# Kernel tuning notes

Measured on AMD Instinct MI355X. Metric: run time of the kernel, lower is better.

Reference implementation:

```python
import jax, jax.numpy as jnp
import numpy as np

N = 50000      # nodes
E = 800000     # edges (avg degree 16)
D = 128        # in_dim
H = 128        # hidden_dim
C = 10         # n_classes
G = 128        # graphs in batch
N_HID = 3      # hidden_layers (total convs = 1 + N_HID)


def setup_inputs() -> dict:
    key = jax.random.key(0)
    ks = jax.random.split(key, 10)
    s = 0.05  # weight init scale
    x = jax.random.normal(ks[0], (N, D), jnp.float32)
    edge_index = jax.random.randint(ks[1], (2, E), 0, N, dtype=jnp.int32)
    graph_ids = jnp.sort(jax.random.randint(ks[2], (N,), 0, G, dtype=jnp.int32))
    W0 = jax.random.normal(ks[3], (D, H), jnp.float32) * s
    b0 = jnp.zeros((H,), jnp.float32)
    Ws = jax.random.normal(ks[4], (N_HID, H, H), jnp.float32) * s
    bs = jnp.zeros((N_HID, H), jnp.float32)
    Wc = jax.random.normal(ks[5], (H, C), jnp.float32) * s
    bc = jnp.zeros((C,), jnp.float32)
    return {"x": x, "W0": W0, "b0": b0, "Ws": Ws, "bs": bs,
            "Wc": Wc, "bc": bc, "edge_index": edge_index, "graph_ids": graph_ids}


def reference(x, W0, b0, Ws, bs, Wc, bc, edge_index, graph_ids):
    src, dst = edge_index[0], edge_index[1]
    ones_e = jnp.ones((E,), x.dtype)
    # DGL GraphConv norm='both': D_out^{-1/2} on source side, D_in^{-1/2} on dest side
    out_deg = jax.ops.segment_sum(ones_e, src, num_segments=N)
    in_deg = jax.ops.segment_sum(ones_e, dst, num_segments=N)
    c_src = jnp.clip(out_deg, 1.0) ** -0.5  # [N]
    c_dst = jnp.clip(in_deg, 1.0) ** -0.5   # [N]

    def conv(h, W, b):
        # h' = relu( c_dst * A (c_src * h) W + b ); dropout is identity in eval mode
        h = h * c_src[:, None]
        m = jax.ops.segment_sum(h[src], dst, num_segments=N)  # gather + scatter-add
        m = m * c_dst[:, None]
        return jax.nn.relu(m @ W + b)

    h = conv(x, W0, b0)
    for i in range(N_HID):  # fixed small layer count
        h = conv(h, Ws[i], bs[i])

    # mean readout per graph
    cnt = jax.ops.segment_sum(jnp.ones((N,), h.dtype), graph_ids, num_segments=G)
    hg = jax.ops.segment_sum(h, graph_ids, num_segments=G) / jnp.clip(cnt, 1.0)[:, None]
    return hg @ Wc + bc  # [G, C]
```

## Files before the change

kernel.cpp:

```cpp
#include <hip/hip_runtime.h>

#define N_NODES 50000
#define N_EDGES 800000
#define DIM     128
#define NGRAPH  128
#define NCLASS  10
#define NLAYER  4

#define TEAMS   256
#define ESLICE  (N_EDGES / TEAMS)
#define CWORDS  12500
#define DUMMY   50000
#define PRE_BLOCKS 12501

typedef __attribute__((ext_vector_type(8))) short short8;
typedef __attribute__((ext_vector_type(4))) float floatx4;

__device__ __forceinline__ unsigned f2bf(float f) {
    union { float f; unsigned u; } v; v.f = f;
    return (v.u + 0x7fffu + ((v.u >> 16) & 1u)) >> 16;
}
__device__ __forceinline__ float bf_lo(unsigned u) { return __uint_as_float(u << 16); }
__device__ __forceinline__ float bf_hi(unsigned u) { return __uint_as_float(u & 0xffff0000u); }

__global__ __launch_bounds__(1024) void count_kernel(
    const int* __restrict__ ei, unsigned* __restrict__ cntw,
    unsigned* __restrict__ colc_fill)
{
    __shared__ unsigned h[CWORDS];
    int team = blockIdx.x, tid = threadIdx.x;
    for (int i = tid; i < CWORDS; i += 1024) h[i] = 0;
    __syncthreads();
    const int e0 = team * ESLICE;
    const int* __restrict__ srcp = ei;
    const int* __restrict__ dstp = ei + N_EDGES;
    for (int e = e0 + tid; e < e0 + ESLICE; e += 1024) {
        int s = srcp[e], d = dstp[e];
        atomicAdd(&h[d >> 2], 1u  << (8 * (d & 3)));
        atomicAdd(&h[s >> 2], 16u << (8 * (s & 3)));
    }
    __syncthreads();
    for (int i = tid; i < CWORDS; i += 1024)
        cntw[(size_t)team * CWORDS + i] = h[i];
    for (int i = blockIdx.x * 1024 + tid; i < N_NODES * 32; i += TEAMS * 1024)
        colc_fill[i] = 0xC350C350u;
}

__global__ __launch_bounds__(1024) void offsets_kernel(
    const unsigned* __restrict__ cntw, unsigned* __restrict__ offsw,
    unsigned* __restrict__ cnt_dense, float* __restrict__ c_src,
    float* __restrict__ c_dst)
{
    __shared__ unsigned ldsC[128 * 64];
    __shared__ unsigned ldsO[128 * 64];
    int tid = threadIdx.x;
    int n0 = blockIdx.x * 256;
    int w0 = n0 >> 2;
    unsigned indeg = 0, outdeg = 0;
    for (int ph = 0; ph < 2; ++ph) {
        int t0 = ph * 128;
        for (int i = tid; i < 128 * 64; i += 1024) {
            int tl = i >> 6, wl = i & 63;
            int gw = w0 + wl;
            ldsC[i] = (gw < CWORDS) ? cntw[(size_t)(t0 + tl) * CWORDS + gw] : 0u;
        }
        __syncthreads();
        if (tid < 256) {
            unsigned char* ob = (unsigned char*)ldsO;
            for (int tl = 0; tl < 128; ++tl) {
                unsigned wv = ldsC[tl * 64 + (tid >> 2)];
                unsigned b = (wv >> (8 * (tid & 3))) & 255u;
                ob[tl * 256 + tid] = (unsigned char)indeg;
                indeg  += (b & 15u);
                outdeg += (b >> 4);
            }
        }
        __syncthreads();
        for (int i = tid; i < 128 * 64; i += 1024) {
            int tl = i >> 6, wl = i & 63;
            int gw = w0 + wl;
            if (gw < CWORDS) offsw[(size_t)(t0 + tl) * CWORDS + gw] = ldsO[i];
        }
        __syncthreads();
    }
    if (tid < 256) {
        int n = n0 + tid;
        if (n < N_NODES) {
            unsigned id_ = indeg, od = outdeg;
            cnt_dense[n] = id_ > 64u ? 64u : id_;
            if (id_ < 1u) id_ = 1u;
            if (od < 1u) od = 1u;
            c_dst[n] = 1.0f / sqrtf((float)id_);
            c_src[n] = 1.0f / sqrtf((float)od);
        }
    }
}

__global__ __launch_bounds__(1024) void scatter_kernel(
    const int* __restrict__ ei, const unsigned* __restrict__ offsw,
    unsigned short* __restrict__ colc)
{
    __shared__ unsigned h[CWORDS];
    int team = blockIdx.x, tid = threadIdx.x;
    for (int i = tid; i < CWORDS; i += 1024) h[i] = 0;
    __syncthreads();
    const unsigned char* __restrict__ ob =
        (const unsigned char*)offsw + (size_t)team * 50000;
    const int e0 = team * ESLICE;
    const int* __restrict__ srcp = ei;
    const int* __restrict__ dstp = ei + N_EDGES;
    for (int e = e0 + tid; e < e0 + ESLICE; e += 1024) {
        int s = srcp[e], d = dstp[e];
        unsigned old = atomicAdd(&h[d >> 2], 1u << (8 * (d & 3)));
        unsigned pos = (old >> (8 * (d & 3))) & 15u;
        unsigned slot = (unsigned)ob[d] + pos;
        if (slot < 64u) colc[(size_t)d * 64 + slot] = (unsigned short)s;
    }
}

__global__ __launch_bounds__(256) void prep_kernel(
    const float2* __restrict__ x, const float* __restrict__ c_src,
    unsigned* __restrict__ hsA, unsigned* __restrict__ hsB,
    const float* __restrict__ W0, const float* __restrict__ Ws,
    uint4* __restrict__ Wf)
{
    int bid = blockIdx.x;
    if (bid < PRE_BLOCKS) {
        int i = bid * 256 + threadIdx.x;
        if (i >= (N_NODES + 1) * 64) return;
        int row = i >> 6;
        if (row < N_NODES) {
            float c = c_src[row];
            float2 v = x[i];
            hsA[i] = f2bf(v.x * c) | (f2bf(v.y * c) << 16);
        } else {
            hsA[i] = 0u;
            hsB[i] = 0u;
        }
        return;
    }
    int t = (bid - PRE_BLOCKS) * 256 + threadIdx.x;
    if (t >= NLAYER * 2048) return;
    int layer = t >> 11;
    int rem = t & 2047;
    int lane = rem & 63;
    int s = (rem >> 6) & 3;
    int c = rem >> 8;
    int quad = lane >> 4, colw = c * 16 + (lane & 15);
    int k0 = s * 32 + quad * 8;
    const float* W = (layer == 0) ? W0 : Ws + (size_t)(layer - 1) * DIM * DIM;
    uint4 p;
    unsigned* pp = (unsigned*)&p;
#pragma unroll
    for (int j = 0; j < 4; ++j) {
        unsigned lo = f2bf(W[(size_t)(k0 + 2 * j) * DIM + colw]);
        unsigned hi = f2bf(W[(size_t)(k0 + 2 * j + 1) * DIM + colw]);
        pp[j] = lo | (hi << 16);
    }
    Wf[t] = p;
}

__global__ __launch_bounds__(256) void layer_kernel(
    const unsigned* __restrict__ hs, const unsigned short* __restrict__ colc,
    const unsigned* __restrict__ cnt_dense, const uint4* __restrict__ Wf,
    const float* __restrict__ bias, const float* __restrict__ c_dst,
    const float* __restrict__ c_src, unsigned short* __restrict__ out_bf,
    float* __restrict__ out_f32, int last)
{
    __shared__ unsigned Ash[16 * 64];
    char* Ab = (char*)Ash;
    int tid = threadIdx.x;
    int wave = tid >> 6, lane = tid & 63;
    int half = lane >> 5, hl = lane & 31;
    unsigned hoff = (unsigned)(hl << 3);
    const char* __restrict__ hb = (const char*)hs;
    int r0 = blockIdx.x * 16;

#pragma unroll
    for (int i = 0; i < 4; ++i) {
        int il = wave * 4 + i;
        int n = r0 + il;
        unsigned deg = cnt_dense[n];
        int myidx = (int)colc[(unsigned)n * 64u + (unsigned)lane];
        float f0 = 0.f, f1 = 0.f, f2 = 0.f, f3 = 0.f;
        for (unsigned j = 0; j < deg; j += 16) {
#pragma unroll
            for (int k = 0; k < 8; ++k) {
                int s = __shfl(myidx, (int)(j + 2u * k) + half);
                uint2 u = *(const uint2*)(hb + (((unsigned)s << 8) + hoff));
                f0 += bf_lo(u.x); f1 += bf_hi(u.x);
                f2 += bf_lo(u.y); f3 += bf_hi(u.y);
            }
        }
        f0 += __shfl_xor(f0, 32); f1 += __shfl_xor(f1, 32);
        f2 += __shfl_xor(f2, 32); f3 += __shfl_xor(f3, 32);
        if (half == 0) {
            uint2 r;
            r.x = f2bf(f0) | (f2bf(f1) << 16);
            r.y = f2bf(f2) | (f2bf(f3) << 16);
            *(uint2*)(Ab + il * 256 + ((hl * 8) ^ ((il & 7) << 4))) = r;
        }
    }
    __syncthreads();

    int quad = lane >> 4, m16 = lane & 15;
    union U { uint4 u; short8 s; };
    U a[4];
#pragma unroll
    for (int s = 0; s < 4; ++s)
        a[s].u = *(const uint4*)(
            Ab + m16 * 256 + ((s * 64 + quad * 16) ^ ((m16 & 7) << 4)));

    floatx4 acc[2];
#pragma unroll
    for (int cc = 0; cc < 2; ++cc) {
        int c = wave * 2 + cc;
        floatx4 ac = {0.f, 0.f, 0.f, 0.f};
#pragma unroll
        for (int s = 0; s < 4; ++s) {
            U b; b.u = Wf[(c * 4 + s) * 64 + lane];
            ac = __builtin_amdgcn_mfma_f32_16x16x32_bf16(a[s].s, b.s, ac, 0, 0, 0);
        }
        acc[cc] = ac;
    }

    float cd[4], cs[4];
#pragma unroll
    for (int r = 0; r < 4; ++r) {
        int row = r0 + quad * 4 + r;
        cd[r] = c_dst[row];
        cs[r] = last ? 1.f : c_src[row];
    }
#pragma unroll
    for (int cc = 0; cc < 2; ++cc) {
        int colg = (wave * 2 + cc) * 16 + m16;
        float b = bias[colg];
#pragma unroll
        for (int r = 0; r < 4; ++r) {
            int row = r0 + quad * 4 + r;
            float v = acc[cc][r] * cd[r] + b;
            v = v > 0.f ? v : 0.f;
            if (last) out_f32[(size_t)row * DIM + colg] = v;
            else      out_bf[(size_t)row * DIM + colg] = (unsigned short)f2bf(v * cs[r]);
        }
    }
}

__global__ __launch_bounds__(128) void readout_kernel(
    const float* __restrict__ h, const int* __restrict__ gid,
    float* __restrict__ hg, float* __restrict__ cntg)
{
    int j  = threadIdx.x;
    int n0 = blockIdx.x * 64;
    float acc = 0.f; int cur = -1; int run = 0;
    for (int i = 0; i < 64; ++i) {
        int n = n0 + i;
        if (n >= N_NODES) break;
        int g = gid[n];
        if (g != cur) {
            if (cur >= 0) {
                atomicAdd(&hg[cur * DIM + j], acc);
                if (j == 0) atomicAdd(&cntg[cur], (float)run);
            }
            cur = g; acc = 0.f; run = 0;
        }
        acc += h[(size_t)n * DIM + j];
        run++;
    }
    if (cur >= 0) {
        atomicAdd(&hg[cur * DIM + j], acc);
        if (j == 0) atomicAdd(&cntg[cur], (float)run);
    }
}

__global__ __launch_bounds__(256) void head_kernel(
    const float* __restrict__ hg, const float* __restrict__ cntg,
    const float* __restrict__ Wc, const float* __restrict__ bc,
    float* __restrict__ out)
{
    int idx = blockIdx.x * blockDim.x + threadIdx.x;
    if (idx >= NGRAPH * NCLASS) return;
    int g = idx / NCLASS, c = idx % NCLASS;
    float inv = 1.0f / fmaxf(cntg[g], 1.0f);
    float s = 0.f;
    for (int j = 0; j < DIM; ++j) s = fmaf(hg[g * DIM + j], Wc[j * NCLASS + c], s);
    out[idx] = s * inv + bc[c];
}

extern "C" void kernel_launch(void* const* d_in, const int* in_sizes, int n_in,
                              void* d_out, int out_size, void* d_ws, size_t ws_size,
                              hipStream_t stream)
{
    const float* x   = (const float*)d_in[0];
    const float* W0  = (const float*)d_in[1];
    const float* b0  = (const float*)d_in[2];
    const float* Ws  = (const float*)d_in[3];
    const float* bs  = (const float*)d_in[4];
    const float* Wc  = (const float*)d_in[5];
    const float* bc  = (const float*)d_in[6];
    const int*   ei  = (const int*)d_in[7];
    const int*   gid = (const int*)d_in[8];
    float* out = (float*)d_out;

    char* ws = (char*)d_ws;
    size_t o = 0;
    auto alloc = [&](size_t bytes) {
        size_t r = o; o = (o + bytes + 255) & ~(size_t)255; return r;
    };
    unsigned* cntw      = (unsigned*)(ws + alloc((size_t)TEAMS * CWORDS * 4));
    unsigned* offsw     = (unsigned*)(ws + alloc((size_t)TEAMS * CWORDS * 4));
    unsigned* cnt_dense = (unsigned*)(ws + alloc((size_t)N_NODES * 4));
    float*    c_src     = (float*)(ws + alloc((size_t)N_NODES * 4));
    float*    c_dst     = (float*)(ws + alloc((size_t)N_NODES * 4));
    unsigned short* colc = (unsigned short*)(ws + alloc((size_t)N_NODES * 64 * 2));
    unsigned* hsA       = (unsigned*)(ws + alloc((size_t)(N_NODES + 1) * 64 * 4));
    unsigned* hsB       = (unsigned*)(ws + alloc((size_t)(N_NODES + 1) * 64 * 4));
    float*    hlast     = (float*)(ws + alloc((size_t)N_NODES * DIM * 4));
    uint4*    Wf        = (uint4*)(ws + alloc((size_t)NLAYER * 2048 * 16));
    float*    hg        = (float*)(ws + alloc((size_t)NGRAPH * DIM * 4));
    float*    cntg      = (float*)(ws + alloc((size_t)NGRAPH * 4));

    hipMemsetAsync(hg,   0, (size_t)NGRAPH * DIM * 4, stream);
    hipMemsetAsync(cntg, 0, (size_t)NGRAPH * 4, stream);

    count_kernel<<<TEAMS, 1024, 0, stream>>>(ei, cntw, (unsigned*)colc);
    offsets_kernel<<<(N_NODES + 255) / 256, 1024, 0, stream>>>(
        cntw, offsw, cnt_dense, c_src, c_dst);
    scatter_kernel<<<TEAMS, 1024, 0, stream>>>(ei, offsw, colc);
    prep_kernel<<<PRE_BLOCKS + (NLAYER * 2048 + 255) / 256, 256, 0, stream>>>(
        (const float2*)x, c_src, hsA, hsB, W0, Ws, Wf);

    const int LAYER_BLOCKS = N_NODES / 16;

    for (int l = 0; l < NLAYER; ++l) {
        const float* b = (l == 0) ? b0 : (bs + (size_t)(l - 1) * DIM);
        int last = (l == NLAYER - 1) ? 1 : 0;
        const unsigned* hin = (l & 1) ? hsB : hsA;
        unsigned* hout      = (l & 1) ? hsA : hsB;
        layer_kernel<<<LAYER_BLOCKS, 256, 0, stream>>>(
            hin, colc, cnt_dense, Wf + (size_t)l * 2048, b, c_dst, c_src,
            (unsigned short*)hout, hlast, last);
    }

    readout_kernel<<<(N_NODES + 63) / 64, 128, 0, stream>>>(hlast, gid, hg, cntg);
    head_kernel<<<(NGRAPH * NCLASS + 255) / 256, 256, 0, stream>>>(hg, cntg, Wc, bc, out);
}
```

Baseline: 284.9 us.

## Build padded adjacency with global atomics and interleave four-node gathers

Replaces the three-pass team-histogram count/offset/scatter pipeline with a single pass. That pass uses global atomicAdd on per-node degree counters to claim slots in the padded column array, followed by a small normalisation kernel. The layer kernel now gathers neighbours for four destination nodes at once in one loop bounded by their maximum degree. This exposes more independent loads per wave. The trade-off is contended global atomics, nondeterministic neighbour order in the column array, and extra gathers of padding entries for lower-degree nodes.

```diff
diff --git a/kernel.cpp b/kernel.cpp
--- a/kernel.cpp
+++ b/kernel.cpp
@@ -7,9 +7,6 @@
 #define NCLASS  10
 #define NLAYER  4
 
-#define TEAMS   256
-#define ESLICE  (N_EDGES / TEAMS)
-#define CWORDS  12500
 #define DUMMY   50000
 #define PRE_BLOCKS 12501
 
@@ -23,99 +20,42 @@
 __device__ __forceinline__ float bf_lo(unsigned u) { return __uint_as_float(u << 16); }
 __device__ __forceinline__ float bf_hi(unsigned u) { return __uint_as_float(u & 0xffff0000u); }
 
-__global__ __launch_bounds__(1024) void count_kernel(
-    const int* __restrict__ ei, unsigned* __restrict__ cntw,
-    unsigned* __restrict__ colc_fill)
-{
-    __shared__ unsigned h[CWORDS];
-    int team = blockIdx.x, tid = threadIdx.x;
-    for (int i = tid; i < CWORDS; i += 1024) h[i] = 0;
-    __syncthreads();
-    const int e0 = team * ESLICE;
-    const int* __restrict__ srcp = ei;
-    const int* __restrict__ dstp = ei + N_EDGES;
-    for (int e = e0 + tid; e < e0 + ESLICE; e += 1024) {
-        int s = srcp[e], d = dstp[e];
-        atomicAdd(&h[d >> 2], 1u  << (8 * (d & 3)));
-        atomicAdd(&h[s >> 2], 16u << (8 * (s & 3)));
-    }
-    __syncthreads();
-    for (int i = tid; i < CWORDS; i += 1024)
-        cntw[(size_t)team * CWORDS + i] = h[i];
-    for (int i = blockIdx.x * 1024 + tid; i < N_NODES * 32; i += TEAMS * 1024)
-        colc_fill[i] = 0xC350C350u;
-}
-
-__global__ __launch_bounds__(1024) void offsets_kernel(
-    const unsigned* __restrict__ cntw, unsigned* __restrict__ offsw,
+__global__ __launch_bounds__(256) void fill_kernel(
+    unsigned* __restrict__ colc_u, unsigned* __restrict__ indeg,
+    unsigned* __restrict__ outdeg)
+{
+    int stride = gridDim.x * 256;
+    for (int i = blockIdx.x * 256 + threadIdx.x; i < N_NODES * 32; i += stride)
+        colc_u[i] = 0xC350C350u;
+    for (int i = blockIdx.x * 256 + threadIdx.x; i < N_NODES; i += stride) {
+        indeg[i] = 0u; outdeg[i] = 0u;
+    }
+}
+
+__global__ __launch_bounds__(256) void build_kernel(
+    const int* __restrict__ ei, unsigned short* __restrict__ colc,
+    unsigned* __restrict__ indeg, unsigned* __restrict__ outdeg)
+{
+    int e = blockIdx.x * 256 + threadIdx.x;
+    int s = ei[e], d = ei[N_EDGES + e];
+    unsigned pos = atomicAdd(&indeg[d], 1u);
+    if (pos < 64u) colc[(unsigned)d * 64u + pos] = (unsigned short)s;
+    atomicAdd(&outdeg[s], 1u);
+}
+
+__global__ __launch_bounds__(256) void norm_kernel(
+    const unsigned* __restrict__ indeg, const unsigned* __restrict__ outdeg,
     unsigned* __restrict__ cnt_dense, float* __restrict__ c_src,
     float* __restrict__ c_dst)
 {
-    __shared__ unsigned ldsC[128 * 64];
-    __shared__ unsigned ldsO[128 * 64];
-    int tid = threadIdx.x;
-    int n0 = blockIdx.x * 256;
-    int w0 = n0 >> 2;
-    unsigned indeg = 0, outdeg = 0;
-    for (int ph = 0; ph < 2; ++ph) {
-        int t0 = ph * 128;
-        for (int i = tid; i < 128 * 64; i += 1024) {
-            int tl = i >> 6, wl = i & 63;
-            int gw = w0 + wl;
-            ldsC[i] = (gw < CWORDS) ? cntw[(size_t)(t0 + tl) * CWORDS + gw] : 0u;
-        }
-        __syncthreads();
-        if (tid < 256) {
-            unsigned char* ob = (unsigned char*)ldsO;
-            for (int tl = 0; tl < 128; ++tl) {
-                unsigned wv = ldsC[tl * 64 + (tid >> 2)];
-                unsigned b = (wv >> (8 * (tid & 3))) & 255u;
-                ob[tl * 256 + tid] = (unsigned char)indeg;
-                indeg  += (b & 15u);
-                outdeg += (b >> 4);
-            }
-        }
-        __syncthreads();
-        for (int i = tid; i < 128 * 64; i += 1024) {
-            int tl = i >> 6, wl = i & 63;
-            int gw = w0 + wl;
-            if (gw < CWORDS) offsw[(size_t)(t0 + tl) * CWORDS + gw] = ldsO[i];
-        }
-        __syncthreads();
-    }
-    if (tid < 256) {
-        int n = n0 + tid;
-        if (n < N_NODES) {
-            unsigned id_ = indeg, od = outdeg;
-            cnt_dense[n] = id_ > 64u ? 64u : id_;
-            if (id_ < 1u) id_ = 1u;
-            if (od < 1u) od = 1u;
-            c_dst[n] = 1.0f / sqrtf((float)id_);
-            c_src[n] = 1.0f / sqrtf((float)od);
-        }
-    }
-}
-
-__global__ __launch_bounds__(1024) void scatter_kernel(
-    const int* __restrict__ ei, const unsigned* __restrict__ offsw,
-    unsigned short* __restrict__ colc)
-{
-    __shared__ unsigned h[CWORDS];
-    int team = blockIdx.x, tid = threadIdx.x;
-    for (int i = tid; i < CWORDS; i += 1024) h[i] = 0;
-    __syncthreads();
-    const unsigned char* __restrict__ ob =
-        (const unsigned char*)offsw + (size_t)team * 50000;
-    const int e0 = team * ESLICE;
-    const int* __restrict__ srcp = ei;
-    const int* __restrict__ dstp = ei + N_EDGES;
-    for (int e = e0 + tid; e < e0 + ESLICE; e += 1024) {
-        int s = srcp[e], d = dstp[e];
-        unsigned old = atomicAdd(&h[d >> 2], 1u << (8 * (d & 3)));
-        unsigned pos = (old >> (8 * (d & 3))) & 15u;
-        unsigned slot = (unsigned)ob[d] + pos;
-        if (slot < 64u) colc[(size_t)d * 64 + slot] = (unsigned short)s;
-    }
+    int n = blockIdx.x * 256 + threadIdx.x;
+    if (n >= N_NODES) return;
+    unsigned id_ = indeg[n], od = outdeg[n];
+    cnt_dense[n] = id_ > 64u ? 64u : id_;
+    if (id_ < 1u) id_ = 1u;
+    if (od < 1u) od = 1u;
+    c_dst[n] = 1.0f / sqrtf((float)id_);
+    c_src[n] = 1.0f / sqrtf((float)od);
 }
 
 __global__ __launch_bounds__(256) void prep_kernel(
@@ -175,29 +115,57 @@
     unsigned hoff = (unsigned)(hl << 3);
     const char* __restrict__ hb = (const char*)hs;
     int r0 = blockIdx.x * 16;
+    int nb = r0 + wave * 4;
+
+    unsigned d0 = cnt_dense[nb + 0], d1 = cnt_dense[nb + 1];
+    unsigned d2 = cnt_dense[nb + 2], d3 = cnt_dense[nb + 3];
+    unsigned mx01 = d0 > d1 ? d0 : d1, mx23 = d2 > d3 ? d2 : d3;
+    unsigned mx = mx01 > mx23 ? mx01 : mx23;
+    int my0 = (int)colc[(unsigned)(nb + 0) * 64u + (unsigned)lane];
+    int my1 = (int)colc[(unsigned)(nb + 1) * 64u + (unsigned)lane];
+    int my2 = (int)colc[(unsigned)(nb + 2) * 64u + (unsigned)lane];
+    int my3 = (int)colc[(unsigned)(nb + 3) * 64u + (unsigned)lane];
+
+    float f[4][4];
+#pragma unroll
+    for (int i = 0; i < 4; ++i)
+#pragma unroll
+        for (int q = 0; q < 4; ++q) f[i][q] = 0.f;
+
+    for (unsigned j = 0; j < mx; j += 16) {
+#pragma unroll
+        for (int k = 0; k < 8; ++k) {
+            int e = (int)j + 2 * k + half;
+            int s0 = __shfl(my0, e);
+            int s1 = __shfl(my1, e);
+            int s2 = __shfl(my2, e);
+            int s3 = __shfl(my3, e);
+            uint2 u0 = *(const uint2*)(hb + (((unsigned)s0 << 8) + hoff));
+            uint2 u1 = *(const uint2*)(hb + (((unsigned)s1 << 8) + hoff));
+            uint2 u2 = *(const uint2*)(hb + (((unsigned)s2 << 8) + hoff));
+            uint2 u3 = *(const uint2*)(hb + (((unsigned)s3 << 8) + hoff));
+            f[0][0] += bf_lo(u0.x); f[0][1] += bf_hi(u0.x);
+            f[0][2] += bf_lo(u0.y); f[0][3] += bf_hi(u0.y);
+            f[1][0] += bf_lo(u1.x); f[1][1] += bf_hi(u1.x);
+            f[1][2] += bf_lo(u1.y); f[1][3] += bf_hi(u1.y);
+            f[2][0] += bf_lo(u2.x); f[2][1] += bf_hi(u2.x);
+            f[2][2] += bf_lo(u2.y); f[2][3] += bf_hi(u2.y);
+            f[3][0] += bf_lo(u3.x); f[3][1] += bf_hi(u3.x);
+            f[3][2] += bf_lo(u3.y); f[3][3] += bf_hi(u3.y);
+        }
+    }
 
 #pragma unroll
     for (int i = 0; i < 4; ++i) {
-        int il = wave * 4 + i;
-        int n = r0 + il;
-        unsigned deg = cnt_dense[n];
-        int myidx = (int)colc[(unsigned)n * 64u + (unsigned)lane];
-        float f0 = 0.f, f1 = 0.f, f2 = 0.f, f3 = 0.f;
-        for (unsigned j = 0; j < deg; j += 16) {
-#pragma unroll
-            for (int k = 0; k < 8; ++k) {
-                int s = __shfl(myidx, (int)(j + 2u * k) + half);
-                uint2 u = *(const uint2*)(hb + (((unsigned)s << 8) + hoff));
-                f0 += bf_lo(u.x); f1 += bf_hi(u.x);
-                f2 += bf_lo(u.y); f3 += bf_hi(u.y);
-            }
-        }
-        f0 += __shfl_xor(f0, 32); f1 += __shfl_xor(f1, 32);
-        f2 += __shfl_xor(f2, 32); f3 += __shfl_xor(f3, 32);
+        float g0 = f[i][0] + __shfl_xor(f[i][0], 32);
+        float g1 = f[i][1] + __shfl_xor(f[i][1], 32);
+        float g2 = f[i][2] + __shfl_xor(f[i][2], 32);
+        float g3 = f[i][3] + __shfl_xor(f[i][3], 32);
         if (half == 0) {
+            int il = wave * 4 + i;
             uint2 r;
-            r.x = f2bf(f0) | (f2bf(f1) << 16);
-            r.y = f2bf(f2) | (f2bf(f3) << 16);
+            r.x = f2bf(g0) | (f2bf(g1) << 16);
+            r.y = f2bf(g2) | (f2bf(g3) << 16);
             *(uint2*)(Ab + il * 256 + ((hl * 8) ^ ((il & 7) << 4))) = r;
         }
     }
@@ -307,8 +275,8 @@
     auto alloc = [&](size_t bytes) {
         size_t r = o; o = (o + bytes + 255) & ~(size_t)255; return r;
     };
-    unsigned* cntw      = (unsigned*)(ws + alloc((size_t)TEAMS * CWORDS * 4));
-    unsigned* offsw     = (unsigned*)(ws + alloc((size_t)TEAMS * CWORDS * 4));
+    unsigned* indeg     = (unsigned*)(ws + alloc((size_t)N_NODES * 4));
+    unsigned* outdeg    = (unsigned*)(ws + alloc((size_t)N_NODES * 4));
     unsigned* cnt_dense = (unsigned*)(ws + alloc((size_t)N_NODES * 4));
     float*    c_src     = (float*)(ws + alloc((size_t)N_NODES * 4));
     float*    c_dst     = (float*)(ws + alloc((size_t)N_NODES * 4));
@@ -323,10 +291,10 @@
     hipMemsetAsync(hg,   0, (size_t)NGRAPH * DIM * 4, stream);
     hipMemsetAsync(cntg, 0, (size_t)NGRAPH * 4, stream);
 
-    count_kernel<<<TEAMS, 1024, 0, stream>>>(ei, cntw, (unsigned*)colc);
-    offsets_kernel<<<(N_NODES + 255) / 256, 1024, 0, stream>>>(
-        cntw, offsw, cnt_dense, c_src, c_dst);
-    scatter_kernel<<<TEAMS, 1024, 0, stream>>>(ei, offsw, colc);
+    fill_kernel<<<2048, 256, 0, stream>>>((unsigned*)colc, indeg, outdeg);
+    build_kernel<<<N_EDGES / 256, 256, 0, stream>>>(ei, colc, indeg, outdeg);
+    norm_kernel<<<(N_NODES + 255) / 256, 256, 0, stream>>>(
+        indeg, outdeg, cnt_dense, c_src, c_dst);
     prep_kernel<<<PRE_BLOCKS + (NLAYER * 2048 + 255) / 256, 256, 0, stream>>>(
         (const float2*)x, c_src, hsA, hsB, W0, Ws, Wf);
 
```

New measurement: 408.2 us. +43.3%, slower.

## Parallelize offsets prefix scan across all threads; use readlane gather in layer kernel

Applied to the files above, without the earlier changes.

The offsets kernel now splits the 128-team running sum across four thread groups, using an in-LDS partial-sum combine instead of leaving only 256 of 1024 threads busy. The layer kernel's neighbour gather now has each lane load one 4-byte slice of a full row. Neighbour indices are read as packed 16-bit pairs broadcast via readlane rather than shfl, which removes the half-wave split and the cross-half reduction. This cuts shuffle/LDS traffic and serial work, at the cost of narrower (32-bit) per-lane loads and two gathers per readlane.

```diff
diff --git a/kernel.cpp b/kernel.cpp
--- a/kernel.cpp
+++ b/kernel.cpp
@@ -53,10 +53,14 @@
 {
     __shared__ unsigned ldsC[128 * 64];
     __shared__ unsigned ldsO[128 * 64];
+    __shared__ unsigned totG[4 * 256];
+    __shared__ unsigned baseW[4 * 64];
     int tid = threadIdx.x;
+    int g = tid >> 8;
+    int n = tid & 255;
     int n0 = blockIdx.x * 256;
     int w0 = n0 >> 2;
-    unsigned indeg = 0, outdeg = 0;
+    unsigned carryIn = 0, carryOut = 0;
     for (int ph = 0; ph < 2; ++ph) {
         int t0 = ph * 128;
         for (int i = tid; i < 128 * 64; i += 1024) {
@@ -65,33 +69,47 @@
             ldsC[i] = (gw < CWORDS) ? cntw[(size_t)(t0 + tl) * CWORDS + gw] : 0u;
         }
         __syncthreads();
-        if (tid < 256) {
+        unsigned locIn = 0, locOut = 0;
+        {
             unsigned char* ob = (unsigned char*)ldsO;
-            for (int tl = 0; tl < 128; ++tl) {
-                unsigned wv = ldsC[tl * 64 + (tid >> 2)];
-                unsigned b = (wv >> (8 * (tid & 3))) & 255u;
-                ob[tl * 256 + tid] = (unsigned char)indeg;
-                indeg  += (b & 15u);
-                outdeg += (b >> 4);
+            for (int tl = g * 32; tl < g * 32 + 32; ++tl) {
+                unsigned wvd = ldsC[tl * 64 + (n >> 2)];
+                unsigned b = (wvd >> (8 * (n & 3))) & 255u;
+                ob[tl * 256 + n] = (unsigned char)locIn;
+                locIn  += (b & 15u);
+                locOut += (b >> 4);
             }
         }
+        totG[g * 256 + n] = locIn | (locOut << 16);
+        __syncthreads();
+        unsigned baseIn = 0, sumIn = 0, sumOut = 0;
+#pragma unroll
+        for (int gg = 0; gg < 4; ++gg) {
+            unsigned t = totG[gg * 256 + n];
+            if (gg < g) baseIn += (t & 0xffffu);
+            sumIn += (t & 0xffffu); sumOut += (t >> 16);
+        }
+        ((unsigned char*)baseW)[g * 256 + n] = (unsigned char)(carryIn + baseIn);
+        carryIn += sumIn; carryOut += sumOut;
         __syncthreads();
         for (int i = tid; i < 128 * 64; i += 1024) {
             int tl = i >> 6, wl = i & 63;
             int gw = w0 + wl;
-            if (gw < CWORDS) offsw[(size_t)(t0 + tl) * CWORDS + gw] = ldsO[i];
+            if (gw < CWORDS)
+                offsw[(size_t)(t0 + tl) * CWORDS + gw] =
+                    ldsO[i] + baseW[(tl >> 5) * 64 + wl];
         }
         __syncthreads();
     }
     if (tid < 256) {
-        int n = n0 + tid;
-        if (n < N_NODES) {
-            unsigned id_ = indeg, od = outdeg;
-            cnt_dense[n] = id_ > 64u ? 64u : id_;
+        int nn = n0 + tid;
+        if (nn < N_NODES) {
+            unsigned id_ = carryIn, od = carryOut;
+            cnt_dense[nn] = id_ > 64u ? 64u : id_;
             if (id_ < 1u) id_ = 1u;
             if (od < 1u) od = 1u;
-            c_dst[n] = 1.0f / sqrtf((float)id_);
-            c_src[n] = 1.0f / sqrtf((float)od);
+            c_dst[nn] = 1.0f / sqrtf((float)id_);
+            c_src[nn] = 1.0f / sqrtf((float)od);
         }
     }
 }
@@ -170,36 +188,34 @@
     __shared__ unsigned Ash[16 * 64];
     char* Ab = (char*)Ash;
     int tid = threadIdx.x;
-    int wave = tid >> 6, lane = tid & 63;
-    int half = lane >> 5, hl = lane & 31;
-    unsigned hoff = (unsigned)(hl << 3);
+    int lane = tid & 63;
+    int wv = __builtin_amdgcn_readfirstlane(tid >> 6);
+    int r0 = blockIdx.x * 16;
+    int nb = r0 + wv * 4;
+    const unsigned* __restrict__ cw = (const unsigned*)colc;
     const char* __restrict__ hb = (const char*)hs;
-    int r0 = blockIdx.x * 16;
+    unsigned loff = (unsigned)(lane << 2);
 
 #pragma unroll
     for (int i = 0; i < 4; ++i) {
-        int il = wave * 4 + i;
-        int n = r0 + il;
+        int n = nb + i;
         unsigned deg = cnt_dense[n];
-        int myidx = (int)colc[(unsigned)n * 64u + (unsigned)lane];
-        float f0 = 0.f, f1 = 0.f, f2 = 0.f, f3 = 0.f;
-        for (unsigned j = 0; j < deg; j += 16) {
-#pragma unroll
-            for (int k = 0; k < 8; ++k) {
-                int s = __shfl(myidx, (int)(j + 2u * k) + half);
-                uint2 u = *(const uint2*)(hb + (((unsigned)s << 8) + hoff));
-                f0 += bf_lo(u.x); f1 += bf_hi(u.x);
-                f2 += bf_lo(u.y); f3 += bf_hi(u.y);
+        unsigned rowv = cw[(unsigned)n * 32u + (unsigned)(lane & 31)];
+        float f0 = 0.f, f1 = 0.f;
+        for (unsigned j = 0; j < deg; j += 8) {
+#pragma unroll
+            for (int k = 0; k < 4; ++k) {
+                unsigned w = (unsigned)__builtin_amdgcn_readlane(
+                    (int)rowv, (int)(j >> 1) + k);
+                unsigned u0 = *(const unsigned*)(hb + ((w & 0xffffu) << 8) + loff);
+                unsigned u1 = *(const unsigned*)(hb + ((w >> 16) << 8) + loff);
+                f0 += bf_lo(u0); f1 += bf_hi(u0);
+                f0 += bf_lo(u1); f1 += bf_hi(u1);
             }
         }
-        f0 += __shfl_xor(f0, 32); f1 += __shfl_xor(f1, 32);
-        f2 += __shfl_xor(f2, 32); f3 += __shfl_xor(f3, 32);
-        if (half == 0) {
-            uint2 r;
-            r.x = f2bf(f0) | (f2bf(f1) << 16);
-            r.y = f2bf(f2) | (f2bf(f3) << 16);
-            *(uint2*)(Ab + il * 256 + ((hl * 8) ^ ((il & 7) << 4))) = r;
-        }
+        int il = wv * 4 + i;
+        *(unsigned*)(Ab + il * 256 + ((lane << 2) ^ ((il & 7) << 4))) =
+            f2bf(f0) | (f2bf(f1) << 16);
     }
     __syncthreads();
 
@@ -214,7 +230,7 @@
     floatx4 acc[2];
 #pragma unroll
     for (int cc = 0; cc < 2; ++cc) {
-        int c = wave * 2 + cc;
+        int c = wv * 2 + cc;
         floatx4 ac = {0.f, 0.f, 0.f, 0.f};
 #pragma unroll
         for (int s = 0; s < 4; ++s) {
@@ -233,7 +249,7 @@
     }
 #pragma unroll
     for (int cc = 0; cc < 2; ++cc) {
-        int colg = (wave * 2 + cc) * 16 + m16;
+        int colg = (wv * 2 + cc) * 16 + m16;
         float b = bias[colg];
 #pragma unroll
         for (int r = 0; r < 4; ++r) {
```

After: 284.1 us. No clear change (-0.3%).
